# Kernel tuning notes

Measured on AMD Instinct MI355X. Metric: run time of the kernel, lower is better.

## Reference

```python
import jax, jax.numpy as jnp
import numpy as np
from jax import lax

H = 2048          # hidden_size
NAH = 16          # num attn heads
AHD = H // NAH    # 128
NFH = 4           # num lact (fast-weight) heads
FHD = H // NFH    # 512 = d_in = d_out
DH = FHD          # d_h = d_in * inter_multi (1.0)
WIN = 1024        # sliding window
CHUNK = 512       # lact chunk size
B, S = 2, 2048
ROPE_BASE = 500000.0
EPS = 1e-6
BASE_LR_INV = 0.001 + float(np.log(-np.expm1(-0.001)))  # inv_softplus(1e-3)


def rms_norm(x, w):
    return x * lax.rsqrt(jnp.mean(x * x, axis=-1, keepdims=True) + EPS) * w


def silu(x):
    return x * jax.nn.sigmoid(x)


def silu_backprop(dy, x):
    sg = jax.nn.sigmoid(x)
    return dy * sg * (1.0 + x * (1.0 - sg))


def apply_rope(q, k):
    # q,k: [b,s,h,d]; non-interleaved (half-split) rotary, matching flash-attn RotaryEmbedding
    d = q.shape[-1]
    inv_freq = 1.0 / (ROPE_BASE ** (jnp.arange(0, d, 2, dtype=jnp.float32) / d))
    t = jnp.arange(q.shape[1], dtype=jnp.float32)
    freqs = jnp.outer(t, inv_freq)                       # [s, d/2]
    cos = jnp.cos(freqs)[None, :, None, :]
    sin = jnp.sin(freqs)[None, :, None, :]
    def rot(x):
        x1, x2 = jnp.split(x, 2, axis=-1)
        return jnp.concatenate([x1 * cos - x2 * sin, x2 * cos + x1 * sin], axis=-1)
    return rot(q), rot(k)


def sliding_window_attn(q, k, v):
    # [b,s,h,d]; causal sliding-window attention
    s = q.shape[1]
    scale = 1.0 / np.sqrt(q.shape[-1])
    i = jnp.arange(s)[:, None]
    j = jnp.arange(s)[None, :]
    mask = (j <= i) & (i - j < WIN)                      # [s,s]
    scores = jnp.einsum('bihd,bjhd->bhij', q, k) * scale
    scores = jnp.where(mask[None, None], scores, -jnp.inf)
    p = jax.nn.softmax(scores, axis=-1)
    return jnp.einsum('bhij,bjhd->bihd', p, v)


def setup_inputs() -> dict:
    key = jax.random.key(0)
    ks = jax.random.split(key, 10)
    def n(k, shape, scale):
        return jax.random.normal(k, shape, dtype=jnp.float32) * scale
    return {
        'hidden_states': n(ks[0], (B, S, H), 1.0),
        'attn_qkv_w': n(ks[1], (3 * H, H), 0.02),
        'attn_o_w': n(ks[2], (H, H), 0.02),
        'q_norm_w': jnp.ones((H,), jnp.float32),
        'k_norm_w': jnp.ones((H,), jnp.float32),
        'mlp_norm_w': jnp.ones((H,), jnp.float32),
        'mlp_qkv_w': n(ks[3], (3 * NFH * FHD, H), 0.02),
        'mlp_o_w': n(ks[4], (H, NFH * FHD), 0.02),
        'lr_w': n(ks[5], (3 * NFH, H), 0.02),
        'lr_b': jnp.zeros((3 * NFH,), jnp.float32),
        'w0': n(ks[6], (NFH, DH, FHD), 1.0 / np.sqrt(FHD)),
        'w1': n(ks[7], (NFH, FHD, DH), 1.0 / np.sqrt(DH)),
        'w2': n(ks[8], (NFH, DH, FHD), 1.0 / np.sqrt(FHD)),
        'ttt_norm_w': jnp.ones((FHD,), jnp.float32),
    }


def _forward(hidden_states, attn_qkv_w, attn_o_w, q_norm_w, k_norm_w, mlp_norm_w,
             mlp_qkv_w, mlp_o_w, lr_w, lr_b, w0, w1, w2, ttt_norm_w):
    b, s, _ = hidden_states.shape
    # ---- sliding window attention (token mixer) ----
    qkv = hidden_states @ attn_qkv_w.T
    q, k, v = jnp.split(qkv, 3, axis=-1)
    q = rms_norm(q, q_norm_w)
    k = rms_norm(k, k_norm_w)
    q = q.reshape(b, s, NAH, AHD)
    k = k.reshape(b, s, NAH, AHD)
    v = v.reshape(b, s, NAH, AHD)
    q, k = apply_rope(q, k)
    o = sliding_window_attn(q, k, v)
    attn_out = o.reshape(b, s, H) @ attn_o_w.T

    # ---- TTT-MLP SwiGLU fast-weight channel mixer after SWA ----
    x = rms_norm(attn_out, mlp_norm_w)
    fqkv = x @ mlp_qkv_w.T
    fq, fk, fv = jnp.split(fqkv, 3, axis=-1)
    fq, fk, fv = silu(fq), silu(fk), silu(fv)
    fq = fq.reshape(b, s, NFH, FHD)
    fk = fk.reshape(b, s, NFH, FHD)
    fv = fv.reshape(b, s, NFH, FHD)
    fq = fq / jnp.clip(jnp.linalg.norm(fq, axis=-1, keepdims=True), 1e-6)
    fk = fk / jnp.clip(jnp.linalg.norm(fk, axis=-1, keepdims=True), 1e-6)

    # per-token lrs (mamba parameterization: softplus(proj + inv_softplus(base_lr)))
    lr = jax.nn.softplus(x @ lr_w.T + lr_b + BASE_LR_INV)   # [b,s,3*NFH]
    l0, l1, l2 = jnp.split(lr, 3, axis=-1)                  # each [b,s,NFH]

    nc = s // CHUNK
    def chunkify(t):  # [b,s,h,d] -> [nc,b,h,c,d]
        return t.reshape(b, nc, CHUNK, t.shape[2], t.shape[3]).transpose(1, 0, 3, 2, 4)
    qs = chunkify(fq)
    ks_ = chunkify(fk)
    vs = chunkify(fv)
    l0s = chunkify(l0[..., None])
    l1s = chunkify(l1[..., None])
    l2s = chunkify(l2[..., None])

    w0b = jnp.broadcast_to(w0[None], (b,) + w0.shape)
    w1b = jnp.broadcast_to(w1[None], (b,) + w1.shape)
    w2b = jnp.broadcast_to(w2[None], (b,) + w2.shape)

    def step(carry, inp):
        cw0, cw1, cw2 = carry
        qc, kc, vc, lr0, lr1, lr2 = inp   # qc/kc/vc: [b,h,c,d]; lr*: [b,h,c,1]
        # apply current fast weights to queries of this chunk (apply-then-update)
        gq = jnp.einsum('bhed,bhcd->bhce', cw0, qc)
        hq = silu(gq) * jnp.einsum('bhed,bhcd->bhce', cw2, qc)
        oc = jnp.einsum('bhoe,bhce->bhco', cw1, hq)
        # update fast weights with this chunk's (k, v) under negative dot-product loss
        gk = jnp.einsum('bhed,bhcd->bhce', cw0, kc)      # gate pre-act
        hbm = jnp.einsum('bhed,bhcd->bhce', cw2, kc)     # hidden before mul
        hid = silu(gk) * hbm
        dhid = jnp.einsum('bhoe,bhco->bhce', cw1, vc)    # grad wrt hidden
        dhbm = dhid * silu(gk)
        dgate = dhid * hbm
        dgpre = silu_backprop(dgate, gk)
        nw1 = cw1 + jnp.einsum('bhco,bhce->bhoe', vc * lr1, hid)
        nw0 = cw0 + jnp.einsum('bhce,bhcd->bhed', dgpre, kc * lr0)
        nw2 = cw2 + jnp.einsum('bhce,bhcd->bhed', dhbm, kc * lr2)
        return (nw0, nw1, nw2), oc

    _, ocs = lax.scan(step, (w0b, w1b, w2b), (qs, ks_, vs, l0s, l1s, l2s))
    o_fw = ocs.transpose(1, 0, 3, 2, 4).reshape(b, s, NFH, FHD)
    o_fw = rms_norm(o_fw, ttt_norm_w)
    ttt_out = o_fw.reshape(b, s, NFH * FHD) @ mlp_o_w.T
    return attn_out + ttt_out


def reference(hidden_states, attn_qkv_w, attn_o_w, q_norm_w, k_norm_w, mlp_norm_w,
              mlp_qkv_w, mlp_o_w, lr_w, lr_b, w0, w1, w2, ttt_norm_w):
    return _forward(hidden_states, attn_qkv_w, attn_o_w, q_norm_w, k_norm_w, mlp_norm_w,
                    mlp_qkv_w, mlp_o_w, lr_w, lr_b, w0, w1, w2, ttt_norm_w)
```

## Files before the change

### kernel.cpp

```cpp
#include <hip/hip_runtime.h>
#include <cmath>

typedef unsigned short u16;
typedef unsigned int u32;
typedef short s16x8 __attribute__((ext_vector_type(8)));
typedef short s16x4 __attribute__((ext_vector_type(4)));
typedef float f32x4 __attribute__((ext_vector_type(4)));

#define DEV static __device__ __forceinline__

DEV float b2f(u16 h) { return __uint_as_float(((u32)h) << 16); }
DEV u16 f2b(float f) {
  u32 u = __float_as_uint(f);
  u = (u + 0x7FFFu + ((u >> 16) & 1u)) >> 16;
  return (u16)u;
}
DEV float siluf(float x) { return x / (1.f + __expf(-x)); }

DEV void gload16(const void* g, void* l) {
  __builtin_amdgcn_global_load_lds((const __attribute__((address_space(1))) void*)g,
                                   (__attribute__((address_space(3))) void*)l, 16, 0, 0);
}

DEV s16x8 lds_frag(const u16* buf, int row, int kg) {
  int lin = row * 64 + kg * 16;
  int adr = lin ^ (((row >> 1) & 3) << 4);
  return *(const s16x8*)((const char*)buf + adr);
}

template <int MODE>
__global__ __launch_bounds__(256, 3) void gemm128(const u16* __restrict__ A, const u16* __restrict__ B,
                                                  void* __restrict__ Cout, const float* __restrict__ Cin,
                                                  int ldc, int K, int gx) {
  __shared__ __align__(16) u16 Al[3][128 * 32];
  __shared__ __align__(16) u16 Bl[3][128 * 32];
  int tid = threadIdx.x, w = tid >> 6, l = tid & 63;
  int cpx = gx >> 3;
  int idx = blockIdx.x >> 3;
  int bx = (blockIdx.x & 7) * cpx + idx % cpx;
  int by = idx / cpx;
  const u16* Ab = A + (long)by * 128 * K;
  const u16* Bb = B + (long)bx * 128 * K;
  int wr = w >> 1, wc = w & 1;
  int fro = l & 15, kg = l >> 4;
  f32x4 acc[4][4] = {};
  int nk = K >> 5;

  auto stage = [&](int buf, int kt) {
    #pragma unroll
    for (int i = 0; i < 2; ++i) {
      int x = (tid + i * 256) * 16;
      int y = x ^ (((x >> 7) & 3) << 4);
      gload16(Ab + (long)(y >> 6) * K + kt * 32 + ((y & 63) >> 1), (char*)&Al[buf][0] + x);
      gload16(Bb + (long)(y >> 6) * K + kt * 32 + ((y & 63) >> 1), (char*)&Bl[buf][0] + x);
    }
  };

  stage(0, 0);
  stage(1, 1);
  asm volatile("s_waitcnt vmcnt(4)" ::: "memory");
  __builtin_amdgcn_s_barrier();

  int cur = 0;
  for (int t = 0; t < nk; ++t) {
    const u16* Ac = &Al[cur][0];
    const u16* Bc = &Bl[cur][0];
    s16x8 af[4], bfr[4];
    #pragma unroll
    for (int m = 0; m < 4; ++m) af[m] = lds_frag(Ac, wr * 64 + m * 16 + fro, kg);
    #pragma unroll
    for (int n = 0; n < 4; ++n) bfr[n] = lds_frag(Bc, wc * 64 + n * 16 + fro, kg);
    if (t + 2 < nk) {
      int nb = cur + 2; if (nb >= 3) nb -= 3;
      stage(nb, t + 2);
    }
    __builtin_amdgcn_s_setprio(1);
    #pragma unroll
    for (int m = 0; m < 4; ++m)
      #pragma unroll
      for (int n = 0; n < 4; ++n)
        acc[m][n] = __builtin_amdgcn_mfma_f32_16x16x32_bf16(af[m], bfr[n], acc[m][n], 0, 0, 0);
    __builtin_amdgcn_s_setprio(0);
    if (t + 2 < nk)      asm volatile("s_waitcnt vmcnt(4)" ::: "memory");
    else if (t + 1 < nk) asm volatile("s_waitcnt vmcnt(0)" ::: "memory");
    __builtin_amdgcn_s_barrier();
    if (++cur == 3) cur = 0;
  }

  long rbase = (long)by * 128 + wr * 64 + kg * 4;
  long cbase = (long)bx * 128 + wc * 64 + fro;
  #pragma unroll
  for (int m = 0; m < 4; ++m)
    #pragma unroll
    for (int n = 0; n < 4; ++n)
      #pragma unroll
      for (int j = 0; j < 4; ++j) {
        long r = rbase + m * 16 + j;
        long c = cbase + n * 16;
        float v = acc[m][n][j];
        if (MODE == 2) v += Cin[r * ldc + c];
        if (MODE == 0) ((u16*)Cout)[r * ldc + c] = f2b(v);
        else ((float*)Cout)[r * ldc + c] = v;
      }
}

struct GemmDesc {
  const u16* A; const u16* B;
  float* C; const float* Cin;
  u16* Cb; u16* CbT;
  long sAb, sAh, sBb, sBh, sCb_, sCh_, sCbb, sCbh, sCtb, sCth;
  int lda, ldb, ldc, ldcb, ldct, K;
};
struct GemmBatch { GemmDesc d[5]; int nbh; };

__global__ __launch_bounds__(256, 3) void gemm_bt(GemmBatch gb) {
  int di = blockIdx.z / gb.nbh;
  int bh = blockIdx.z % gb.nbh;
  GemmDesc d = gb.d[di];
  __shared__ __align__(16) u16 As[3][4096];
  __shared__ __align__(16) u16 Bs[3][4096];
  int tid = threadIdx.x, w = tid >> 6, l = tid & 63;
  int b2 = bh >> 2, h2 = bh & 3;
  const u16* Ab = d.A + (long)b2 * d.sAb + (long)h2 * d.sAh + (long)blockIdx.y * 128 * d.lda;
  const u16* Bb = d.B + (long)b2 * d.sBb + (long)h2 * d.sBh + (long)blockIdx.x * 128 * d.ldb;
  f32x4 acc[4][4] = {};
  int nk = d.K >> 5;

  auto stage = [&](int buf, int kt) {
    #pragma unroll
    for (int i = 0; i < 2; ++i) {
      int x = (tid + i * 256) * 16;
      int y = x ^ (((x >> 7) & 3) << 4);
      gload16(Ab + (long)(y >> 6) * d.lda + kt * 32 + ((y & 63) >> 1), (char*)&As[buf][0] + x);
      gload16(Bb + (long)(y >> 6) * d.ldb + kt * 32 + ((y & 63) >> 1), (char*)&Bs[buf][0] + x);
    }
  };

  stage(0, 0);
  stage(1, 1);
  asm volatile("s_waitcnt vmcnt(4)" ::: "memory");
  __builtin_amdgcn_s_barrier();

  int wr = (w >> 1) * 64, wc = (w & 1) * 64;
  int fro = l & 15, kg = l >> 4;

  int cur = 0;
  for (int kt = 0; kt < nk; ++kt) {
    const u16* Ac = &As[cur][0];
    const u16* Bc = &Bs[cur][0];
    s16x8 af[4], bfr[4];
    #pragma unroll
    for (int m = 0; m < 4; ++m) af[m] = lds_frag(Ac, wr + m * 16 + fro, kg);
    #pragma unroll
    for (int n = 0; n < 4; ++n) bfr[n] = lds_frag(Bc, wc + n * 16 + fro, kg);
    if (kt + 2 < nk) {
      int nb = cur + 2; if (nb >= 3) nb -= 3;
      stage(nb, kt + 2);
    }
    __builtin_amdgcn_s_setprio(1);
    #pragma unroll
    for (int m = 0; m < 4; ++m)
      #pragma unroll
      for (int n = 0; n < 4; ++n)
        acc[m][n] = __builtin_amdgcn_mfma_f32_16x16x32_bf16(af[m], bfr[n], acc[m][n], 0, 0, 0);
    __builtin_amdgcn_s_setprio(0);
    if (kt + 2 < nk)      asm volatile("s_waitcnt vmcnt(4)" ::: "memory");
    else if (kt + 1 < nk) asm volatile("s_waitcnt vmcnt(0)" ::: "memory");
    __builtin_amdgcn_s_barrier();
    if (++cur == 3) cur = 0;
  }

  float* Cp = d.C ? d.C + (long)b2 * d.sCb_ + (long)h2 * d.sCh_ : nullptr;
  const float* Ci = d.Cin ? d.Cin + (long)b2 * d.sCb_ + (long)h2 * d.sCh_ : nullptr;
  u16* Cbp = d.Cb ? d.Cb + (long)b2 * d.sCbb + (long)h2 * d.sCbh : nullptr;
  u16* Ctp = d.CbT ? d.CbT + (long)b2 * d.sCtb + (long)h2 * d.sCth : nullptr;
  long rbase = (long)blockIdx.y * 128 + wr + kg * 4;
  long cbase = (long)blockIdx.x * 128 + wc + fro;
  #pragma unroll
  for (int m = 0; m < 4; ++m)
    #pragma unroll
    for (int n = 0; n < 4; ++n)
      #pragma unroll
      for (int j = 0; j < 4; ++j) {
        long r = rbase + m * 16 + j;
        long c = cbase + n * 16;
        float v = acc[m][n][j];
        if (Ci) v += Ci[r * d.ldc + c];
        if (Cp) Cp[r * d.ldc + c] = v;
        if (Cbp) Cbp[r * d.ldcb + c] = f2b(v);
        if (Ctp) Ctp[c * d.ldct + r] = f2b(v);
      }
}

__global__ __launch_bounds__(256) void convk(const float* __restrict__ in, u16* __restrict__ outp) {
  long i = ((long)blockIdx.x * 256 + threadIdx.x) * 4;
  float4 v = *(const float4*)(in + i);
  u16 o[4] __attribute__((aligned(8))) = {f2b(v.x), f2b(v.y), f2b(v.z), f2b(v.w)};
  *(s16x4*)&outp[i] = *(const s16x4*)o;
}

__global__ __launch_bounds__(256) void norm_rope_kernel(const u16* __restrict__ qkv,
    const float* __restrict__ qw, const float* __restrict__ kw,
    u16* __restrict__ qg, u16* __restrict__ kg, u16* __restrict__ vg) {
  __shared__ float qsh[2048], ksh[2048];
  __shared__ float red[2][4];
  int t = blockIdx.x, tid = threadIdx.x, w = tid >> 6, l = tid & 63;
  int s = t & 2047;
  const u16* row = qkv + (long)t * 6144;
  s16x8 vq = *(const s16x8*)&row[tid * 8];
  s16x8 vk = *(const s16x8*)&row[2048 + tid * 8];
  float sq = 0.f, sk = 0.f;
  #pragma unroll
  for (int i = 0; i < 8; ++i) {
    float a = b2f((u16)vq[i]); qsh[tid * 8 + i] = a; sq += a * a;
    float c = b2f((u16)vk[i]); ksh[tid * 8 + i] = c; sk += c * c;
  }
  *(s16x8*)&vg[(long)t * 2048 + tid * 8] = *(const s16x8*)&row[4096 + tid * 8];
  #pragma unroll
  for (int mk = 32; mk; mk >>= 1) { sq += __shfl_xor(sq, mk, 64); sk += __shfl_xor(sk, mk, 64); }
  if (l == 0) { red[0][w] = sq; red[1][w] = sk; }
  __syncthreads();
  float rq = rsqrtf((red[0][0] + red[0][1] + red[0][2] + red[0][3]) * (1.f / 2048.f) + 1e-6f);
  float rk = rsqrtf((red[1][0] + red[1][1] + red[1][2] + red[1][3]) * (1.f / 2048.f) + 1e-6f);
  const float lf = 13.122363377404329f / 64.f;
  #pragma unroll
  for (int ii = 0; ii < 4; ++ii) {
    int pid = tid + 256 * ii;
    int h = pid >> 6, dpos = pid & 63;
    float invf = expf(-(float)dpos * lf);
    float ang = (float)s * invf;
    float sn, cs;
    sincosf(ang, &sn, &cs);
    int i1 = h * 128 + dpos, i2 = i1 + 64;
    float q1 = qsh[i1] * rq * qw[i1], q2 = qsh[i2] * rq * qw[i2];
    qg[(long)t * 2048 + i1] = f2b(q1 * cs - q2 * sn);
    qg[(long)t * 2048 + i2] = f2b(q2 * cs + q1 * sn);
    float k1 = ksh[i1] * rk * kw[i1], k2v = ksh[i2] * rk * kw[i2];
    kg[(long)t * 2048 + i1] = f2b(k1 * cs - k2v * sn);
    kg[(long)t * 2048 + i2] = f2b(k2v * cs + k1 * sn);
  }
}

__global__ __launch_bounds__(256) void vtrans_kernel(const u16* __restrict__ v, u16* __restrict__ vT) {
  __shared__ u16 T[64][74];
  int tid = threadIdx.x;
  int bh = blockIdx.z, b = bh >> 4, h = bh & 15;
  int ts = blockIdx.x * 64, dg = blockIdx.y * 64;
  int r = tid >> 2, c0 = (tid & 3) * 16;
  const u16* src = v + ((long)b * 2048 + ts + r) * 2048 + h * 128 + dg + c0;
  *(s16x8*)&T[r][c0] = *(const s16x8*)src;
  *(s16x8*)&T[r][c0 + 8] = *(const s16x8*)(src + 8);
  __syncthreads();
  int d = tid >> 2, tg = (tid & 3) * 16;
  u16 a[16] __attribute__((aligned(16)));
  #pragma unroll
  for (int j = 0; j < 16; ++j) a[j] = T[tg + j][d];
  u16* dst = vT + ((long)bh * 128 + dg + d) * 2048 + ts + tg;
  *(s16x8*)dst = ((const s16x8*)a)[0];
  *(s16x8*)(dst + 8) = ((const s16x8*)a)[1];
}

__global__ __launch_bounds__(256, 2) void attn_kernel(const u16* __restrict__ qg, const u16* __restrict__ kg,
                                                      const u16* __restrict__ vT, u16* __restrict__ og) {
  __shared__ __align__(16) u16 Ks[64][136];
  __shared__ __align__(16) u16 Vt[128][72];
  __shared__ __align__(16) u16 Ps[4][32][72];
  int tid = threadIdx.x, w = tid >> 6, l = tid & 63;
  int h = blockIdx.y, b = blockIdx.z;
  int xs = ((blockIdx.x & 7) << 1) | (blockIdx.x >> 3);
  int qs = xs * 128;
  long tokb = (long)b * 2048;
  int fr = l & 15, fg = l >> 4;
  int wrow = qs + w * 32;

  s16x8 qf[2][4];
  #pragma unroll
  for (int rt = 0; rt < 2; ++rt)
    #pragma unroll
    for (int ks = 0; ks < 4; ++ks)
      qf[rt][ks] = *(const s16x8*)&qg[(tokb + wrow + rt * 16 + fr) * 2048 + h * 128 + ks * 32 + fg * 8];

  f32x4 oacc[2][8] = {};
  float mrun[2][4], lrun[2][4];
  #pragma unroll
  for (int rt = 0; rt < 2; ++rt)
    #pragma unroll
    for (int j = 0; j < 4; ++j) { mrun[rt][j] = -__builtin_inff(); lrun[rt][j] = 0.f; }

  int lo = qs - 1023;
  int t0 = lo > 0 ? (lo >> 6) : 0;
  int t1 = (qs + 127) >> 6;
  const float scale = 0.088388347648318447f;

  const u16* kbase = kg + tokb * 2048 + h * 128;
  const u16* vbase = vT + (long)(b * 16 + h) * 128 * 2048;

  s16x8 kreg[4], vreg[4];
  auto loadrg = [&](int kvs) {
    #pragma unroll
    for (int it = 0; it < 4; ++it) {
      int idx = it * 256 + tid;
      kreg[it] = *(const s16x8*)&kbase[(long)(kvs + (idx >> 4)) * 2048 + (idx & 15) * 8];
      vreg[it] = *(const s16x8*)&vbase[(long)(idx >> 3) * 2048 + kvs + (idx & 7) * 8];
    }
  };
  auto writelds = [&]() {
    #pragma unroll
    for (int it = 0; it < 4; ++it) {
      int idx = it * 256 + tid;
      *(s16x8*)&Ks[idx >> 4][(idx & 15) * 8] = kreg[it];
      *(s16x8*)&Vt[idx >> 3][(idx & 7) * 8] = vreg[it];
    }
  };

  loadrg(t0 << 6);
  writelds();
  __syncthreads();

  for (int kt = t0; kt <= t1; ++kt) {
    int kvs = kt << 6;
    if (kt < t1) loadrg((kt + 1) << 6);
    bool active = (kvs <= wrow + 31);
    if (active) {
      f32x4 st[2][4] = {};
      #pragma unroll
      for (int ct = 0; ct < 4; ++ct)
        #pragma unroll
        for (int ks = 0; ks < 4; ++ks) {
          s16x8 kf = *(const s16x8*)&Ks[ct * 16 + fr][ks * 32 + fg * 8];
          st[0][ct] = __builtin_amdgcn_mfma_f32_16x16x32_bf16(qf[0][ks], kf, st[0][ct], 0, 0, 0);
          st[1][ct] = __builtin_amdgcn_mfma_f32_16x16x32_bf16(qf[1][ks], kf, st[1][ct], 0, 0, 0);
        }
      bool needm = (kvs + 63 > wrow) || (kvs < wrow - 992);
      #pragma unroll
      for (int rt = 0; rt < 2; ++rt) {
        float mx[4];
        #pragma unroll
        for (int j = 0; j < 4; ++j) mx[j] = -__builtin_inff();
        #pragma unroll
        for (int ct = 0; ct < 4; ++ct)
          #pragma unroll
          for (int j = 0; j < 4; ++j) {
            float s = st[rt][ct][j] * scale;
            if (needm) {
              int r = wrow + rt * 16 + fg * 4 + j;
              int c = kvs + ct * 16 + fr;
              if (c > r || (r - c) >= 1024) s = -__builtin_inff();
            }
            st[rt][ct][j] = s;
            mx[j] = fmaxf(mx[j], s);
          }
        #pragma unroll
        for (int mk = 8; mk; mk >>= 1)
          #pragma unroll
          for (int j = 0; j < 4; ++j) mx[j] = fmaxf(mx[j], __shfl_xor(mx[j], mk, 64));
        float sc[4], nmu[4], rs[4];
        #pragma unroll
        for (int j = 0; j < 4; ++j) {
          float nm = fmaxf(mrun[rt][j], mx[j]);
          nmu[j] = (nm == -__builtin_inff()) ? 0.f : nm;
          sc[j] = __expf(mrun[rt][j] - nmu[j]);
          mrun[rt][j] = nm;
          rs[j] = 0.f;
        }
        #pragma unroll
        for (int ct = 0; ct < 4; ++ct)
          #pragma unroll
          for (int j = 0; j < 4; ++j) {
            float p = __expf(st[rt][ct][j] - nmu[j]);
            rs[j] += p;
            Ps[w][rt * 16 + fg * 4 + j][ct * 16 + fr] = f2b(p);
          }
        #pragma unroll
        for (int mk = 8; mk; mk >>= 1)
          #pragma unroll
          for (int j = 0; j < 4; ++j) rs[j] += __shfl_xor(rs[j], mk, 64);
        #pragma unroll
        for (int j = 0; j < 4; ++j) lrun[rt][j] = lrun[rt][j] * sc[j] + rs[j];
        #pragma unroll
        for (int dt = 0; dt < 8; ++dt)
          #pragma unroll
          for (int j = 0; j < 4; ++j) oacc[rt][dt][j] *= sc[j];
      }
      #pragma unroll
      for (int kst = 0; kst < 2; ++kst) {
        s16x8 pf0 = *(const s16x8*)&Ps[w][fr][kst * 32 + fg * 8];
        s16x8 pf1 = *(const s16x8*)&Ps[w][16 + fr][kst * 32 + fg * 8];
        #pragma unroll
        for (int dt = 0; dt < 8; ++dt) {
          s16x8 vf = *(const s16x8*)&Vt[dt * 16 + fr][kst * 32 + fg * 8];
          oacc[0][dt] = __builtin_amdgcn_mfma_f32_16x16x32_bf16(pf0, vf, oacc[0][dt], 0, 0, 0);
          oacc[1][dt] = __builtin_amdgcn_mfma_f32_16x16x32_bf16(pf1, vf, oacc[1][dt], 0, 0, 0);
        }
      }
    }
    __syncthreads();
    if (kt < t1) {
      writelds();
    }
    __syncthreads();
  }
  #pragma unroll
  for (int rt = 0; rt < 2; ++rt)
    #pragma unroll
    for (int j = 0; j < 4; ++j) {
      float inv = 1.f / lrun[rt][j];
      long rofs = (tokb + wrow + rt * 16 + fg * 4 + j) * 2048 + h * 128;
      #pragma unroll
      for (int dt = 0; dt < 8; ++dt)
        og[rofs + dt * 16 + fr] = f2b(oacc[rt][dt][j] * inv);
    }
}

__global__ __launch_bounds__(256) void rms_x_kernel(const float* __restrict__ src, const float* __restrict__ wgt,
                                                    u16* __restrict__ dst) {
  __shared__ float red[4];
  int t = blockIdx.x, tid = threadIdx.x, w = tid >> 6, l = tid & 63;
  const float* row = src + (long)t * 2048;
  float v[8] __attribute__((aligned(16)));
  ((float4*)v)[0] = *(const float4*)&row[tid * 8];
  ((float4*)v)[1] = *(const float4*)&row[tid * 8 + 4];
  float ss = 0.f;
  #pragma unroll
  for (int i = 0; i < 8; ++i) ss += v[i] * v[i];
  #pragma unroll
  for (int mk = 32; mk; mk >>= 1) ss += __shfl_xor(ss, mk, 64);
  if (l == 0) red[w] = ss;
  __syncthreads();
  float r = rsqrtf((red[0] + red[1] + red[2] + red[3]) * (1.f / 2048.f) + 1e-6f);
  #pragma unroll
  for (int i = 0; i < 8; ++i) dst[(long)t * 2048 + tid * 8 + i] = f2b(v[i] * r * wgt[tid * 8 + i]);
}

__global__ __launch_bounds__(256) void lr_kernel(const u16* __restrict__ xb, const float* __restrict__ lrw,
                                                 const float* __restrict__ lrbias, float* __restrict__ lrout,
                                                 float base) {
  __shared__ float red[4][12];
  int t = blockIdx.x, tid = threadIdx.x, w = tid >> 6, l = tid & 63;
  float xv[8];
  s16x8 rv = *(const s16x8*)&xb[(long)t * 2048 + tid * 8];
  #pragma unroll
  for (int i = 0; i < 8; ++i) xv[i] = b2f((u16)rv[i]);
  float acc[12];
  #pragma unroll
  for (int j = 0; j < 12; ++j) {
    const float4* w4 = (const float4*)(lrw + j * 2048 + tid * 8);
    float4 a = w4[0], bq = w4[1];
    acc[j] = xv[0] * a.x + xv[1] * a.y + xv[2] * a.z + xv[3] * a.w +
             xv[4] * bq.x + xv[5] * bq.y + xv[6] * bq.z + xv[7] * bq.w;
  }
  #pragma unroll
  for (int j = 0; j < 12; ++j)
    #pragma unroll
    for (int mk = 32; mk; mk >>= 1) acc[j] += __shfl_xor(acc[j], mk, 64);
  if (l == 0) {
    #pragma unroll
    for (int j = 0; j < 12; ++j) red[w][j] = acc[j];
  }
  __syncthreads();
  if (tid < 12) {
    float s_ = red[0][tid] + red[1][tid] + red[2][tid] + red[3][tid] + lrbias[tid] + base;
    lrout[(long)t * 12 + tid] = (s_ > 20.f) ? s_ : log1pf(__expf(s_));
  }
}

__global__ __launch_bounds__(256) void silu_norm_kernel(const u16* __restrict__ fqkv,
    u16* __restrict__ fqo, u16* __restrict__ fko, u16* __restrict__ fvo) {
  int t = blockIdx.x, tid = threadIdx.x, w = tid >> 6, l = tid & 63;
  const u16* row = fqkv + (long)t * 6144;
  {
    s16x8 rv = *(const s16x8*)&row[w * 512 + l * 8];
    float x[8]; float ss = 0.f;
    #pragma unroll
    for (int i = 0; i < 8; ++i) { x[i] = siluf(b2f((u16)rv[i])); ss += x[i] * x[i]; }
    #pragma unroll
    for (int mk = 32; mk; mk >>= 1) ss += __shfl_xor(ss, mk, 64);
    float sc = 1.f / fmaxf(sqrtf(ss), 1e-6f);
    #pragma unroll
    for (int i = 0; i < 8; ++i) fqo[(long)t * 2048 + w * 512 + l * 8 + i] = f2b(x[i] * sc);
  }
  {
    s16x8 rv = *(const s16x8*)&row[2048 + w * 512 + l * 8];
    float x[8]; float ss = 0.f;
    #pragma unroll
    for (int i = 0; i < 8; ++i) { x[i] = siluf(b2f((u16)rv[i])); ss += x[i] * x[i]; }
    #pragma unroll
    for (int mk = 32; mk; mk >>= 1) ss += __shfl_xor(ss, mk, 64);
    float sc = 1.f / fmaxf(sqrtf(ss), 1e-6f);
    #pragma unroll
    for (int i = 0; i < 8; ++i) fko[(long)t * 2048 + w * 512 + l * 8 + i] = f2b(x[i] * sc);
  }
  {
    s16x8 rv = *(const s16x8*)&row[4096 + tid * 8];
    #pragma unroll
    for (int i = 0; i < 8; ++i) fvo[(long)t * 2048 + tid * 8 + i] = f2b(siluf(b2f((u16)rv[i])));
  }
}

__global__ __launch_bounds__(256) void winit_kernel(const float* __restrict__ w0, const float* __restrict__ w1,
                                                    const float* __restrict__ w2,
                                                    float* __restrict__ wbuf0, u16* __restrict__ wb16) {
  long gid = (long)blockIdx.x * 256 + threadIdx.x;
  long e4 = gid * 4;
  int which = (int)(e4 >> 21);
  long rem = e4 & 2097151L;
  int bh = (int)(rem >> 18);
  long idx = rem & 262143L;
  int h = bh & 3;
  const float* src = (which == 0 ? w0 : which == 1 ? w1 : w2) + (long)h * 262144 + idx;
  float4 v = *(const float4*)src;
  *(float4*)(wbuf0 + e4) = v;
  u16 o[4] __attribute__((aligned(8))) = {f2b(v.x), f2b(v.y), f2b(v.z), f2b(v.w)};
  *(s16x4*)&wb16[e4] = *(const s16x4*)o;
  if (which == 1) {
    u16* wt = wb16 + 3L * 2097152 + (long)bh * 262144;
    int r = (int)(idx >> 9), c = (int)(idx & 511);
    wt[(long)(c + 0) * 512 + r] = o[0];
    wt[(long)(c + 1) * 512 + r] = o[1];
    wt[(long)(c + 2) * 512 + r] = o[2];
    wt[(long)(c + 3) * 512 + r] = o[3];
  }
}

__global__ __launch_bounds__(256) void ttt_elem_kernel(
    const float* __restrict__ t5, u16* __restrict__ hqb,
    u16* __restrict__ hidT, u16* __restrict__ dhbmT, u16* __restrict__ dgpT,
    const u16* __restrict__ fk, const u16* __restrict__ fv, const float* __restrict__ lr,
    u16* __restrict__ k0T, u16* __restrict__ k2T, u16* __restrict__ v1T, int ic) {
  __shared__ u16 T0[64][72], T1[64][72], T2[64][72];
  int tid = threadIdx.x;
  int bh = blockIdx.y, b = bh >> 2, h = bh & 3;
  int tc = (blockIdx.x >> 3) * 64, te = (blockIdx.x & 7) * 64;
  int r = tid >> 2, c0 = (tid & 3) * 16;
  long base = (long)bh * 262144 + (long)(tc + r) * 512 + te + c0;

  {
    float gq_[16] __attribute__((aligned(16)));
    float q2_[16] __attribute__((aligned(16)));
    const float* pgq = t5 + base;
    const float* pq2 = t5 + 2097152L + base;
    #pragma unroll
    for (int q4 = 0; q4 < 4; ++q4) {
      ((float4*)gq_)[q4] = *(const float4*)(pgq + q4 * 4);
      ((float4*)q2_)[q4] = *(const float4*)(pq2 + q4 * 4);
    }
    u16 hq_[16] __attribute__((aligned(16)));
    #pragma unroll
    for (int i = 0; i < 16; ++i) hq_[i] = f2b(siluf(gq_[i]) * q2_[i]);
    *(s16x8*)&hqb[base] = ((const s16x8*)hq_)[0];
    *(s16x8*)&hqb[base + 8] = ((const s16x8*)hq_)[1];
  }
  {
    float gk_[16] __attribute__((aligned(16)));
    float k2_[16] __attribute__((aligned(16)));
    float dh_[16] __attribute__((aligned(16)));
    const float* pgk = t5 + 2L * 2097152 + base;
    const float* pk2 = t5 + 3L * 2097152 + base;
    const float* pdh = t5 + 4L * 2097152 + base;
    #pragma unroll
    for (int q4 = 0; q4 < 4; ++q4) {
      ((float4*)gk_)[q4] = *(const float4*)(pgk + q4 * 4);
      ((float4*)k2_)[q4] = *(const float4*)(pk2 + q4 * 4);
      ((float4*)dh_)[q4] = *(const float4*)(pdh + q4 * 4);
    }
    #pragma unroll
    for (int i = 0; i < 16; ++i) {
      float sg = 1.f / (1.f + __expf(-gk_[i]));
      float sil = gk_[i] * sg;
      float hid = sil * k2_[i];
      float dhbm = dh_[i] * sil;
      float dgate = dh_[i] * k2_[i];
      float dgp = dgate * sg * (1.f + gk_[i] * (1.f - sg));
      T0[r][c0 + i] = f2b(hid);
      T1[r][c0 + i] = f2b(dhbm);
      T2[r][c0 + i] = f2b(dgp);
    }
  }
  __syncthreads();
  long obase = (long)bh * 262144 + (long)(te + r) * 512 + tc + c0;
  {
    u16 a0[16] __attribute__((aligned(16))), a1[16] __attribute__((aligned(16))), a2[16] __attribute__((aligned(16)));
    #pragma unroll
    for (int i = 0; i < 16; ++i) { a0[i] = T0[c0 + i][r]; a1[i] = T1[c0 + i][r]; a2[i] = T2[c0 + i][r]; }
    *(s16x8*)&hidT[obase] = ((const s16x8*)a0)[0];   *(s16x8*)&hidT[obase + 8] = ((const s16x8*)a0)[1];
    *(s16x8*)&dhbmT[obase] = ((const s16x8*)a1)[0];  *(s16x8*)&dhbmT[obase + 8] = ((const s16x8*)a1)[1];
    *(s16x8*)&dgpT[obase] = ((const s16x8*)a2)[0];   *(s16x8*)&dgpT[obase + 8] = ((const s16x8*)a2)[1];
  }
  __syncthreads();
  {
    long to = (long)b * 2048 + (long)ic * 512 + tc + r;
    float l0 = lr[to * 12 + h], l1 = lr[to * 12 + 4 + h], l2 = lr[to * 12 + 8 + h];
    long goff = to * 2048 + (long)h * 512 + te + c0;
    s16x8 ka = *(const s16x8*)&fk[goff];
    s16x8 kb8 = *(const s16x8*)&fk[goff + 8];
    s16x8 va = *(const s16x8*)&fv[goff];
    s16x8 vb8 = *(const s16x8*)&fv[goff + 8];
    #pragma unroll
    for (int i = 0; i < 8; ++i) {
      float kv1 = b2f((u16)ka[i]), kv2 = b2f((u16)kb8[i]);
      float vv1 = b2f((u16)va[i]), vv2 = b2f((u16)vb8[i]);
      T0[r][c0 + i] = f2b(kv1 * l0);      T0[r][c0 + 8 + i] = f2b(kv2 * l0);
      T1[r][c0 + i] = f2b(kv1 * l2);      T1[r][c0 + 8 + i] = f2b(kv2 * l2);
      T2[r][c0 + i] = f2b(vv1 * l1);      T2[r][c0 + 8 + i] = f2b(vv2 * l1);
    }
  }
  __syncthreads();
  {
    u16 a0[16] __attribute__((aligned(16))), a1[16] __attribute__((aligned(16))), a2[16] __attribute__((aligned(16)));
    #pragma unroll
    for (int i = 0; i < 16; ++i) { a0[i] = T0[c0 + i][r]; a1[i] = T1[c0 + i][r]; a2[i] = T2[c0 + i][r]; }
    *(s16x8*)&k0T[obase] = ((const s16x8*)a0)[0];  *(s16x8*)&k0T[obase + 8] = ((const s16x8*)a0)[1];
    *(s16x8*)&k2T[obase] = ((const s16x8*)a1)[0];  *(s16x8*)&k2T[obase + 8] = ((const s16x8*)a1)[1];
    *(s16x8*)&v1T[obase] = ((const s16x8*)a2)[0];  *(s16x8*)&v1T[obase + 8] = ((const s16x8*)a2)[1];
  }
}

__global__ __launch_bounds__(256) void ttt_norm_kernel(const u16* __restrict__ src, const float* __restrict__ wgt,
                                                       u16* __restrict__ dst) {
  int t = blockIdx.x, tid = threadIdx.x, w = tid >> 6, l = tid & 63;
  long off = (long)t * 2048 + w * 512 + l * 8;
  s16x8 rv = *(const s16x8*)&src[off];
  float x[8];
  float ss = 0.f;
  #pragma unroll
  for (int i = 0; i < 8; ++i) { x[i] = b2f((u16)rv[i]); ss += x[i] * x[i]; }
  #pragma unroll
  for (int mk = 32; mk; mk >>= 1) ss += __shfl_xor(ss, mk, 64);
  float r = rsqrtf(ss * (1.f / 512.f) + 1e-6f);
  #pragma unroll
  for (int i = 0; i < 8; ++i) dst[off + i] = f2b(x[i] * r * wgt[l * 8 + i]);
}

extern "C" void kernel_launch(void* const* d_in, const int* in_sizes, int n_in,
                              void* d_out, int out_size, void* d_ws, size_t ws_size,
                              hipStream_t stream) {
  const float* hidden     = (const float*)d_in[0];
  const float* attn_qkv_w = (const float*)d_in[1];
  const float* attn_o_w   = (const float*)d_in[2];
  const float* q_norm_w   = (const float*)d_in[3];
  const float* k_norm_w   = (const float*)d_in[4];
  const float* mlp_norm_w = (const float*)d_in[5];
  const float* mlp_qkv_w  = (const float*)d_in[6];
  const float* mlp_o_w    = (const float*)d_in[7];
  const float* lr_w       = (const float*)d_in[8];
  const float* lr_bias    = (const float*)d_in[9];
  const float* w0in       = (const float*)d_in[10];
  const float* w1in       = (const float*)d_in[11];
  const float* w2in       = (const float*)d_in[12];
  const float* ttt_w      = (const float*)d_in[13];
  float* out = (float*)d_out;

  char* ws = (char*)d_ws;
  u16* hbf   = (u16*)(ws + 0);
  u16* wqb   = (u16*)(ws + 16777216);
  u16* wob   = (u16*)(ws + 41943040);
  char* big  = ws + 50331648;
  u16* qbuf  = (u16*)(ws + 121634816);
  u16* kbuf  = (u16*)(ws + 138412032);
  u16* vbuf  = (u16*)(ws + 155189248);
  u16* obuf  = (u16*)(ws + 171966464);
  float* lrb_ = (float*)(ws + 188743680);
  float* wbuf = (float*)(ws + 188940288);
  u16* wb16  = (u16*)(ws + 239271936);

  u16* qkvb = (u16*)big;
  u16* vTb  = (u16*)(big + 50331648);
  float* t5 = (float*)big;
  u16* hqb   = (u16*)(big + 41943040);
  u16* hidT  = (u16*)(big + 46137344);
  u16* dhbmT = (u16*)(big + 50331648);
  u16* dgpT  = (u16*)(big + 54525952);
  u16* k0T   = (u16*)(big + 58720256);
  u16* k2T   = (u16*)(big + 62914560);
  u16* v1T   = (u16*)(big + 67108864);
  u16* xb  = hbf;
  u16* ofw = hbf;

  convk<<<8192, 256, 0, stream>>>(hidden, hbf);
  convk<<<12288, 256, 0, stream>>>(attn_qkv_w, wqb);
  convk<<<4096, 256, 0, stream>>>(attn_o_w, wob);

  gemm128<0><<<1536, 256, 0, stream>>>(hbf, wqb, qkvb, nullptr, 6144, 2048, 48);
  norm_rope_kernel<<<4096, 256, 0, stream>>>(qkvb, q_norm_w, k_norm_w, qbuf, kbuf, vbuf);
  vtrans_kernel<<<dim3(32, 2, 32), 256, 0, stream>>>(vbuf, vTb);
  attn_kernel<<<dim3(16, 16, 2), 256, 0, stream>>>(qbuf, kbuf, vTb, obuf);
  gemm128<1><<<512, 256, 0, stream>>>(obuf, wob, out, nullptr, 2048, 2048, 16);
  rms_x_kernel<<<4096, 256, 0, stream>>>(out, mlp_norm_w, xb);
  convk<<<12288, 256, 0, stream>>>(mlp_qkv_w, wqb);
  convk<<<4096, 256, 0, stream>>>(mlp_o_w, wob);
  float base_lr_inv = 0.001f + logf(-expm1f(-0.001f));
  lr_kernel<<<4096, 256, 0, stream>>>(xb, lr_w, lr_bias, lrb_, base_lr_inv);
  gemm128<0><<<1536, 256, 0, stream>>>(xb, wqb, qkvb, nullptr, 6144, 2048, 48);
  silu_norm_kernel<<<4096, 256, 0, stream>>>(qkvb, qbuf, kbuf, vbuf);
  winit_kernel<<<6144, 256, 0, stream>>>(w0in, w1in, w2in, wbuf, wb16);

  for (int ic = 0; ic < 4; ++ic) {
    {
      GemmBatch g{}; g.nbh = 8;
      const u16* Asrc[5] = {qbuf, qbuf, kbuf, kbuf, vbuf};
      long Bwhich[5] = {0, 2, 0, 2, 3};
      for (int i = 0; i < 5; ++i) {
        GemmDesc& dd = g.d[i];
        dd.A = Asrc[i] + (long)ic * 1048576; dd.sAb = 4194304; dd.sAh = 512; dd.lda = 2048;
        dd.B = wb16 + Bwhich[i] * 2097152;   dd.sBb = 1048576; dd.sBh = 262144; dd.ldb = 512;
        dd.C = t5 + (long)i * 2097152;       dd.sCb_ = 1048576; dd.sCh_ = 262144; dd.ldc = 512;
        dd.K = 512;
      }
      gemm_bt<<<dim3(4, 4, 40), 256, 0, stream>>>(g);
    }
    ttt_elem_kernel<<<dim3(64, 8), 256, 0, stream>>>(t5, hqb, hidT, dhbmT, dgpT,
                                                     kbuf, vbuf, lrb_, k0T, k2T, v1T, ic);
    {
      GemmBatch g{}; g.nbh = 8;
      GemmDesc& dd = g.d[0];
      dd.A = hqb; dd.sAb = 1048576; dd.sAh = 262144; dd.lda = 512;
      dd.B = wb16 + 2097152; dd.sBb = 1048576; dd.sBh = 262144; dd.ldb = 512;
      dd.Cb = ofw + (long)ic * 1048576; dd.sCbb = 4194304; dd.sCbh = 512; dd.ldcb = 2048;
      dd.K = 512;
      gemm_bt<<<dim3(4, 4, 8), 256, 0, stream>>>(g);
    }
    {
      GemmBatch g{}; g.nbh = 8;
      float* wc_ = wbuf + (long)(ic & 1) * 6291456;
      float* wn_ = wbuf + (long)((ic & 1) ^ 1) * 6291456;
      const u16* A3[3] = {dgpT, v1T, dhbmT};
      const u16* B3[3] = {k0T, hidT, k2T};
      for (int i = 0; i < 3; ++i) {
        GemmDesc& dd = g.d[i];
        dd.A = A3[i]; dd.sAb = 1048576; dd.sAh = 262144; dd.lda = 512;
        dd.B = B3[i]; dd.sBb = 1048576; dd.sBh = 262144; dd.ldb = 512;
        dd.Cin = wc_ + (long)i * 2097152; dd.C = wn_ + (long)i * 2097152;
        dd.sCb_ = 1048576; dd.sCh_ = 262144; dd.ldc = 512;
        dd.Cb = wb16 + (long)i * 2097152; dd.sCbb = 1048576; dd.sCbh = 262144; dd.ldcb = 512;
        if (i == 1) { dd.CbT = wb16 + 3L * 2097152; dd.sCtb = 1048576; dd.sCth = 262144; dd.ldct = 512; }
        dd.K = 512;
      }
      gemm_bt<<<dim3(4, 4, 24), 256, 0, stream>>>(g);
    }
  }
  ttt_norm_kernel<<<4096, 256, 0, stream>>>(ofw, ttt_w, obuf);
  gemm128<2><<<512, 256, 0, stream>>>(obuf, wob, out, out, 2048, 2048, 16);
  (void)in_sizes; (void)n_in; (void)out_size; (void)ws_size;
}
```

Measured before the change: 959.8 us.

## Add 256x256 deep-pipelined QKV GEMM and merge output GEMM into weight-update batch

Introduces a 512-thread GEMM kernel with 256x256 tiles and a 4-stage LDS pipeline, used for both QKV projections in place of the 128x128 kernel. The larger tiles raise arithmetic intensity and cut global traffic, but give fewer blocks (384) and lower occupancy. Separately, the per-chunk fast-weight output GEMM is folded into the same batched launch as the three weight-update GEMMs, removing one launch per chunk. Folding them together is only safe if the output GEMM reads the old bf16 w1 before the update GEMMs overwrite it within that launch, which creates a possible race.

```diff
diff --git a/kernel.cpp b/kernel.cpp
--- a/kernel.cpp
+++ b/kernel.cpp
@@ -26,6 +26,86 @@
   int lin = row * 64 + kg * 16;
   int adr = lin ^ (((row >> 1) & 3) << 4);
   return *(const s16x8*)((const char*)buf + adr);
+}
+
+template <int MODE>
+__global__ __launch_bounds__(512, 1) void gemm_deep(const u16* __restrict__ A, const u16* __restrict__ B,
+                                                    void* __restrict__ Cout, const float* __restrict__ Cin,
+                                                    int ldc, int K, int gx) {
+  __shared__ __align__(16) u16 Al[4][256 * 32];
+  __shared__ __align__(16) u16 Bl[4][256 * 32];
+  int tid = threadIdx.x, w = tid >> 6, l = tid & 63;
+  int cpx = gx >> 3;
+  int idx = blockIdx.x >> 3;
+  int bx = (blockIdx.x & 7) * cpx + idx % cpx;
+  int by = idx / cpx;
+  const u16* Ab = A + (long)by * 256 * K;
+  const u16* Bb = B + (long)bx * 256 * K;
+  int wr = w >> 2, wc = w & 3;
+  int fro = l & 15, kg = l >> 4;
+  f32x4 acc[8][4] = {};
+  int nk = K >> 5;
+
+  auto stage = [&](int buf, int kt) {
+    #pragma unroll
+    for (int i = 0; i < 2; ++i) {
+      int x = (tid + i * 512) * 16;
+      int y = x ^ (((x >> 7) & 3) << 4);
+      gload16(Ab + (long)(y >> 6) * K + kt * 32 + ((y & 63) >> 1), (char*)&Al[buf][0] + x);
+    }
+    #pragma unroll
+    for (int i = 0; i < 2; ++i) {
+      int x = (tid + i * 512) * 16;
+      int y = x ^ (((x >> 7) & 3) << 4);
+      gload16(Bb + (long)(y >> 6) * K + kt * 32 + ((y & 63) >> 1), (char*)&Bl[buf][0] + x);
+    }
+  };
+
+  stage(0, 0);
+  stage(1, 1);
+  stage(2, 2);
+  asm volatile("s_waitcnt vmcnt(8)" ::: "memory");
+  __builtin_amdgcn_s_barrier();
+
+  int cur = 0;
+  for (int t = 0; t < nk; ++t) {
+    const u16* Ac = &Al[cur][0];
+    const u16* Bc = &Bl[cur][0];
+    s16x8 af[8], bfr[4];
+    #pragma unroll
+    for (int m = 0; m < 8; ++m) af[m] = lds_frag(Ac, wr * 128 + m * 16 + fro, kg);
+    #pragma unroll
+    for (int n = 0; n < 4; ++n) bfr[n] = lds_frag(Bc, wc * 64 + n * 16 + fro, kg);
+    if (t + 3 < nk) stage((cur + 3) & 3, t + 3);
+    __builtin_amdgcn_s_setprio(1);
+    #pragma unroll
+    for (int m = 0; m < 8; ++m)
+      #pragma unroll
+      for (int n = 0; n < 4; ++n)
+        acc[m][n] = __builtin_amdgcn_mfma_f32_16x16x32_bf16(af[m], bfr[n], acc[m][n], 0, 0, 0);
+    __builtin_amdgcn_s_setprio(0);
+    if (t + 3 < nk)      asm volatile("s_waitcnt vmcnt(8)" ::: "memory");
+    else if (t + 2 < nk) asm volatile("s_waitcnt vmcnt(4)" ::: "memory");
+    else if (t + 1 < nk) asm volatile("s_waitcnt vmcnt(0)" ::: "memory");
+    __builtin_amdgcn_s_barrier();
+    cur = (cur + 1) & 3;
+  }
+
+  long rbase = (long)by * 256 + wr * 128 + kg * 4;
+  long cbase = (long)bx * 256 + wc * 64 + fro;
+  #pragma unroll
+  for (int m = 0; m < 8; ++m)
+    #pragma unroll
+    for (int n = 0; n < 4; ++n)
+      #pragma unroll
+      for (int j = 0; j < 4; ++j) {
+        long r = rbase + m * 16 + j;
+        long c = cbase + n * 16;
+        float v = acc[m][n][j];
+        if (MODE == 2) v += Cin[r * ldc + c];
+        if (MODE == 0) ((u16*)Cout)[r * ldc + c] = f2b(v);
+        else ((float*)Cout)[r * ldc + c] = v;
+      }
 }
 
 template <int MODE>
@@ -680,7 +760,7 @@
   convk<<<12288, 256, 0, stream>>>(attn_qkv_w, wqb);
   convk<<<4096, 256, 0, stream>>>(attn_o_w, wob);
 
-  gemm128<0><<<1536, 256, 0, stream>>>(hbf, wqb, qkvb, nullptr, 6144, 2048, 48);
+  gemm_deep<0><<<384, 512, 0, stream>>>(hbf, wqb, qkvb, nullptr, 6144, 2048, 24);
   norm_rope_kernel<<<4096, 256, 0, stream>>>(qkvb, q_norm_w, k_norm_w, qbuf, kbuf, vbuf);
   vtrans_kernel<<<dim3(32, 2, 32), 256, 0, stream>>>(vbuf, vTb);
   attn_kernel<<<dim3(16, 16, 2), 256, 0, stream>>>(qbuf, kbuf, vTb, obuf);
@@ -690,7 +770,7 @@
   convk<<<4096, 256, 0, stream>>>(mlp_o_w, wob);
   float base_lr_inv = 0.001f + logf(-expm1f(-0.001f));
   lr_kernel<<<4096, 256, 0, stream>>>(xb, lr_w, lr_bias, lrb_, base_lr_inv);
-  gemm128<0><<<1536, 256, 0, stream>>>(xb, wqb, qkvb, nullptr, 6144, 2048, 48);
+  gemm_deep<0><<<384, 512, 0, stream>>>(xb, wqb, qkvb, nullptr, 6144, 2048, 24);
   silu_norm_kernel<<<4096, 256, 0, stream>>>(qkvb, qbuf, kbuf, vbuf);
   winit_kernel<<<6144, 256, 0, stream>>>(w0in, w1in, w2in, wbuf, wb16);
 
@@ -712,21 +792,19 @@
                                                      kbuf, vbuf, lrb_, k0T, k2T, v1T, ic);
     {
       GemmBatch g{}; g.nbh = 8;
-      GemmDesc& dd = g.d[0];
-      dd.A = hqb; dd.sAb = 1048576; dd.sAh = 262144; dd.lda = 512;
-      dd.B = wb16 + 2097152; dd.sBb = 1048576; dd.sBh = 262144; dd.ldb = 512;
-      dd.Cb = ofw + (long)ic * 1048576; dd.sCbb = 4194304; dd.sCbh = 512; dd.ldcb = 2048;
-      dd.K = 512;
-      gemm_bt<<<dim3(4, 4, 8), 256, 0, stream>>>(g);
-    }
-    {
-      GemmBatch g{}; g.nbh = 8;
       float* wc_ = wbuf + (long)(ic & 1) * 6291456;
       float* wn_ = wbuf + (long)((ic & 1) ^ 1) * 6291456;
+      {
+        GemmDesc& dd = g.d[0];
+        dd.A = hqb; dd.sAb = 1048576; dd.sAh = 262144; dd.lda = 512;
+        dd.B = wb16 + 2097152; dd.sBb = 1048576; dd.sBh = 262144; dd.ldb = 512;
+        dd.Cb = ofw + (long)ic * 1048576; dd.sCbb = 4194304; dd.sCbh = 512; dd.ldcb = 2048;
+        dd.K = 512;
+      }
       const u16* A3[3] = {dgpT, v1T, dhbmT};
       const u16* B3[3] = {k0T, hidT, k2T};
       for (int i = 0; i < 3; ++i) {
-        GemmDesc& dd = g.d[i];
+        GemmDesc& dd = g.d[1 + i];
         dd.A = A3[i]; dd.sAb = 1048576; dd.sAh = 262144; dd.lda = 512;
         dd.B = B3[i]; dd.sBb = 1048576; dd.sBh = 262144; dd.ldb = 512;
         dd.Cin = wc_ + (long)i * 2097152; dd.C = wn_ + (long)i * 2097152;
@@ -735,7 +813,7 @@
         if (i == 1) { dd.CbT = wb16 + 3L * 2097152; dd.sCtb = 1048576; dd.sCth = 262144; dd.ldct = 512; }
         dd.K = 512;
       }
-      gemm_bt<<<dim3(4, 4, 24), 256, 0, stream>>>(g);
+      gemm_bt<<<dim3(4, 4, 32), 256, 0, stream>>>(g);
     }
   }
   ttt_norm_kernel<<<4096, 256, 0, stream>>>(ofw, ttt_w, obuf);
```

Result: faster. 908.5 us (-5.3%).
